# Kernel optimization log

Measured on AMD Instinct MI355X. Metric: run time of the kernel, lower is better.

The kernel has to match this reference:

```python
import jax, jax.numpy as jnp
import numpy as np

B, T, D_IN, D_FEAT, D_LAT = 256, 512, 128, 256, 512

def setup_inputs() -> dict:
    key = jax.random.key(0)
    ks = jax.random.split(key, 6)
    s = lambda fan_in: 1.0 / np.sqrt(fan_in)
    return {
        "x": jax.random.normal(ks[0], (B, T, D_IN), dtype=jnp.float32),
        "W_enc": jax.random.normal(ks[1], (D_IN, D_FEAT), dtype=jnp.float32) * s(D_IN),
        "b_enc": jnp.zeros((D_FEAT,), dtype=jnp.float32),
        "W_x": jax.random.normal(ks[2], (D_FEAT, 4 * D_LAT), dtype=jnp.float32) * s(D_FEAT),
        "W_h": jax.random.normal(ks[3], (D_LAT, 4 * D_LAT), dtype=jnp.float32) * s(D_LAT),
        "b_lstm": jnp.zeros((4 * D_LAT,), dtype=jnp.float32),
        "W_dec": jax.random.normal(ks[4], (D_LAT, 1), dtype=jnp.float32) * s(D_LAT),
        "b_dec": jnp.zeros((1,), dtype=jnp.float32),
    }

def reference(x, W_enc, b_enc, W_x, W_h, b_lstm, W_dec, b_dec):
    # Dense encoder with tanh: [B,T,D_IN] -> [B,T,D_FEAT]
    enc = jnp.tanh(jnp.einsum("bti,if->btf", x, W_enc) + b_enc)
    d = W_h.shape[0]
    # Precompute input-to-gate projection for all steps (hoisted out of loop)
    xz = jnp.einsum("btf,fg->btg", enc, W_x) + b_lstm  # [B,T,4d]
    xz_t = jnp.swapaxes(xz, 0, 1)  # [T,B,4d] for scan

    def step(carry, xz_step):
        h, c = carry
        z = xz_step + h @ W_h  # [B,4d]
        i, f, g, o = jnp.split(z, 4, axis=-1)  # Keras gate order: i,f,c,o
        i = jax.nn.sigmoid(i)
        f = jax.nn.sigmoid(f)
        g = jnp.tanh(g)
        o = jax.nn.sigmoid(o)
        c_new = f * c + i * g
        h_new = o * jnp.tanh(c_new)
        return (h_new, c_new), None

    h0 = jnp.zeros((x.shape[0], d), dtype=x.dtype)
    c0 = jnp.zeros((x.shape[0], d), dtype=x.dtype)
    (h_last, _), _ = jax.lax.scan(step, (h0, c0), xz_t)
    # Decoder on last hidden state: [B,d] -> [B,1]
    return h_last @ W_dec + b_dec
```

## Files before the change

### kernel.cpp

```cpp
#include <hip/hip_runtime.h>

#define BATCH 256
#define TLEN  512
#define DIN   128
#define DFEAT 256
#define DLAT  512
#define G4    2048
#define KCAT  768

typedef __bf16 bf16x8 __attribute__((ext_vector_type(8)));
typedef float f32x4 __attribute__((ext_vector_type(4)));

#define WCAT_OFF   0u
#define WENC_OFF   3145728u
#define ENC_OFF    3211264u
#define H_OFF      70320128u
#define FLAG_OFF   70844416u

__device__ __forceinline__ float sigf(float x)  { return 1.0f / (1.0f + __expf(-x)); }
__device__ __forceinline__ float tanhfast(float x){ return 2.0f / (1.0f + __expf(-2.0f * x)) - 1.0f; }
__device__ __forceinline__ unsigned short bfb(float f) {
    __bf16 b = (__bf16)f;
    return __builtin_bit_cast(unsigned short, b);
}

__global__ __launch_bounds__(256) void wprep_kernel(const float* __restrict__ Wx,
                                                    const float* __restrict__ Wh,
                                                    const float* __restrict__ Wenc,
                                                    __bf16* __restrict__ wcat,
                                                    __bf16* __restrict__ wencf) {
    int cid = blockIdx.x * 256 + threadIdx.x;
    float v[8];
    __bf16* dst;
    if (cid < 196608) {
        int widx = cid / 12288;
        int r1 = cid % 12288;
        int nn = r1 / 1536;
        int r2 = r1 % 1536;
        int ks = r2 >> 6, l = r2 & 63;
        int np = nn >> 1, nf = nn & 1;
        int cc = l & 15;
        int gate = (cc < 8) ? (nf ? 2 : 0) : (nf ? 3 : 1);
        int col = gate * 512 + widx * 32 + np * 8 + (cc & 7);
        int kc = ks * 32 + (l >> 4) * 8;
#pragma unroll
        for (int j = 0; j < 8; ++j) {
            int kk = kc + j;
            v[j] = (kk < DFEAT) ? Wx[kk * G4 + col] : Wh[(kk - DFEAT) * G4 + col];
        }
        dst = wcat + (size_t)cid * 8;
    } else {
        int c2 = cid - 196608;
        int ntg = c2 >> 8;
        int r = c2 & 255;
        int ks = r >> 6, l = r & 63;
        int col = ntg * 16 + (l & 15);
        int kc = ks * 32 + (l >> 4) * 8;
#pragma unroll
        for (int j = 0; j < 8; ++j) v[j] = Wenc[(kc + j) * DFEAT + col];
        dst = wencf + (size_t)c2 * 8;
    }
    bf16x8 o;
#pragma unroll
    for (int j = 0; j < 8; ++j) o[j] = (__bf16)v[j];
    *reinterpret_cast<bf16x8*>(dst) = o;
}

__global__ __launch_bounds__(256) void enc_kernel(const float* __restrict__ x,
                                                  const float* __restrict__ benc,
                                                  const __bf16* __restrict__ wencf,
                                                  __bf16* __restrict__ enc) {
    __shared__ uint4 afrag4[1024];
    __bf16* afrag = reinterpret_cast<__bf16*>(afrag4);
    int tid = threadIdx.x;
    int lane = tid & 63, w = tid >> 6;
    int rid0 = blockIdx.x * 64;
    int ntg0 = blockIdx.y * 4;

    bf16x8 wr[4][4];
#pragma unroll
    for (int n = 0; n < 4; ++n)
#pragma unroll
        for (int ks = 0; ks < 4; ++ks)
            wr[n][ks] = *reinterpret_cast<const bf16x8*>(
                wencf + (size_t)(((ntg0 + n) * 4 + ks) * 64 + lane) * 8);
    float bias[4];
#pragma unroll
    for (int n = 0; n < 4; ++n) bias[n] = benc[(ntg0 + n) * 16 + (lane & 15)];

#pragma unroll
    for (int i = 0; i < 4; ++i) {
        int c = tid + 256 * i;
        int row = c >> 4, k8 = c & 15;
        const float* src = x + (size_t)(rid0 + row) * DIN + k8 * 8;
        float4 f0 = *reinterpret_cast<const float4*>(src);
        float4 f1 = *reinterpret_cast<const float4*>(src + 4);
        bf16x8 o;
        o[0] = (__bf16)f0.x; o[1] = (__bf16)f0.y; o[2] = (__bf16)f0.z; o[3] = (__bf16)f0.w;
        o[4] = (__bf16)f1.x; o[5] = (__bf16)f1.y; o[6] = (__bf16)f1.z; o[7] = (__bf16)f1.w;
        int l = (k8 & 3) * 16 + (row & 15);
        int a16 = ((row >> 4) * 4 + (k8 >> 2)) * 64 + l;
        *reinterpret_cast<bf16x8*>(afrag + (size_t)a16 * 8) = o;
    }
    __syncthreads();

    int m = w;
    f32x4 acc[4];
#pragma unroll
    for (int n = 0; n < 4; ++n) acc[n] = (f32x4){bias[n], bias[n], bias[n], bias[n]};
#pragma unroll
    for (int ks = 0; ks < 4; ++ks) {
        bf16x8 a = *reinterpret_cast<const bf16x8*>(afrag + (size_t)((m * 4 + ks) * 64 + lane) * 8);
#pragma unroll
        for (int n = 0; n < 4; ++n)
            acc[n] = __builtin_amdgcn_mfma_f32_16x16x32_bf16(a, wr[n][ks], acc[n], 0, 0, 0);
    }
#pragma unroll
    for (int n = 0; n < 4; ++n) {
        int colg = (ntg0 + n) * 16 + (lane & 15);
#pragma unroll
        for (int q = 0; q < 4; ++q) {
            int rid = rid0 + m * 16 + (lane >> 4) * 4 + q;
            int bb = rid >> 9, tt = rid & 511;
            float th = tanhfast(acc[n][q]);
            enc[(size_t)(tt * BATCH + bb) * DFEAT + colg] = (__bf16)th;
        }
    }
}

__global__ __launch_bounds__(256, 1) void lstm_kernel(const __bf16* __restrict__ enc,
                                                      const __bf16* __restrict__ wcat,
                                                      const float* __restrict__ blstm,
                                                      __bf16* __restrict__ hbuf,
                                                      unsigned int* __restrict__ flags) {
    extern __shared__ char smem[];
    __bf16* afrag = reinterpret_cast<__bf16*>(smem);

    int tid = threadIdx.x;
    int lane = tid & 63, np = tid >> 6;
    int grp = blockIdx.x & 15, widx = blockIdx.x >> 4;
    int b0 = grp * 16;
    unsigned int* myflag = &flags[(grp * 16 + widx) * 16];

    bf16x8 wreg[2][24];
#pragma unroll
    for (int nf = 0; nf < 2; ++nf)
#pragma unroll
        for (int ks = 0; ks < 24; ++ks)
            wreg[nf][ks] = *reinterpret_cast<const bf16x8*>(
                wcat + (size_t)(((((widx * 4 + np) * 2 + nf) * 24) + ks) * 64 + lane) * 8);

    const int cbase = widx * 32 + np * 8 + (lane & 7);
    const bool lo = (lane & 15) < 8;
    const float bias0 = blstm[(lo ? 0 : 1) * 512 + cbase];
    const float bias1 = blstm[(lo ? 2 : 3) * 512 + cbase];

    float c0 = 0.f, c1 = 0.f;
    const int srow = (lane >> 4) * 4 + (lo ? 0 : 2) + (lane & 1);
    const int scol = widx * 32 + np * 8 + (lane & 6);
    unsigned* hdA = reinterpret_cast<unsigned*>(
        hbuf + (size_t)(b0 + srow) * DLAT + scol);
    unsigned* hdB = reinterpret_cast<unsigned*>(
        hbuf + (size_t)BATCH * DLAT + (size_t)(b0 + srow) * DLAT + scol);

#pragma unroll 1
    for (int t = 0; t < TLEN; ++t) {
#pragma unroll
        for (int i = 0; i < 2; ++i) {
            int c = tid + 256 * i;
            int ks = c >> 6, l = c & 63;
            int row = l & 15;
            int k = ks * 32 + (l >> 4) * 8;
            uint4 d = *reinterpret_cast<const uint4*>(
                enc + (size_t)(t * BATCH + b0 + row) * DFEAT + k);
            *reinterpret_cast<uint4*>(afrag + (size_t)c * 8) = d;
        }
        __syncthreads();

        f32x4 acc0 = (f32x4){bias0, bias0, bias0, bias0};
        f32x4 acc1 = (f32x4){bias1, bias1, bias1, bias1};
#pragma unroll
        for (int ks = 0; ks < 8; ++ks) {
            bf16x8 a = *reinterpret_cast<const bf16x8*>(
                afrag + (size_t)((ks * 64 + lane) * 8));
            acc0 = __builtin_amdgcn_mfma_f32_16x16x32_bf16(a, wreg[0][ks], acc0, 0, 0, 0);
            acc1 = __builtin_amdgcn_mfma_f32_16x16x32_bf16(a, wreg[1][ks], acc1, 0, 0, 0);
        }

        if (t > 0) {
            if (tid < 64) {
                const unsigned int* f = &flags[(grp * 16 + (lane & 15)) * 16];
                unsigned v;
                do {
                    v = __hip_atomic_load(f, __ATOMIC_RELAXED, __HIP_MEMORY_SCOPE_AGENT);
                } while (!__all((int)(v >= (unsigned)t)));
            }
            __syncthreads();

            {
                const __bf16* hsrc = hbuf + (size_t)(t & 1) * (BATCH * DLAT);
                const __bf16* src[4];
                int cdst[4];
#pragma unroll
                for (int ii = 0; ii < 4; ++ii) {
                    int c = tid + 256 * (ii + 2);
                    int ks = c >> 6, l = c & 63;
                    int row = l & 15;
                    int kh = ks * 32 + (l >> 4) * 8 - DFEAT;
                    src[ii] = hsrc + (size_t)(b0 + row) * DLAT + kh;
                    cdst[ii] = c;
                }
                uint4 d0, d1, d2, d3;
                asm volatile(
                    "global_load_dwordx4 %0, %4, off sc1\n\t"
                    "global_load_dwordx4 %1, %5, off sc1\n\t"
                    "global_load_dwordx4 %2, %6, off sc1\n\t"
                    "global_load_dwordx4 %3, %7, off sc1\n\t"
                    "s_waitcnt vmcnt(0)"
                    : "=&v"(d0), "=&v"(d1), "=&v"(d2), "=&v"(d3)
                    : "v"(src[0]), "v"(src[1]), "v"(src[2]), "v"(src[3])
                    : "memory");
                *reinterpret_cast<uint4*>(afrag + (size_t)cdst[0] * 8) = d0;
                *reinterpret_cast<uint4*>(afrag + (size_t)cdst[1] * 8) = d1;
                *reinterpret_cast<uint4*>(afrag + (size_t)cdst[2] * 8) = d2;
                *reinterpret_cast<uint4*>(afrag + (size_t)cdst[3] * 8) = d3;
            }
            __syncthreads();

#pragma unroll
            for (int ks = 8; ks < 24; ++ks) {
                bf16x8 a = *reinterpret_cast<const bf16x8*>(
                    afrag + (size_t)((ks * 64 + lane) * 8));
                acc0 = __builtin_amdgcn_mfma_f32_16x16x32_bf16(a, wreg[0][ks], acc0, 0, 0, 0);
                acc1 = __builtin_amdgcn_mfma_f32_16x16x32_bf16(a, wreg[1][ks], acc1, 0, 0, 0);
            }
        }

        float p00 = __shfl_xor(acc0[0], 8), p01 = __shfl_xor(acc0[1], 8);
        float p02 = __shfl_xor(acc0[2], 8), p03 = __shfl_xor(acc0[3], 8);
        float p10 = __shfl_xor(acc1[0], 8), p11 = __shfl_xor(acc1[1], 8);
        float p12 = __shfl_xor(acc1[2], 8), p13 = __shfl_xor(acc1[3], 8);

        float zi_a = lo ? acc0[0] : p02, zf_a = lo ? p00 : acc0[2];
        float zg_a = lo ? acc1[0] : p12, zo_a = lo ? p10 : acc1[2];
        float zi_b = lo ? acc0[1] : p03, zf_b = lo ? p01 : acc0[3];
        float zg_b = lo ? acc1[1] : p13, zo_b = lo ? p11 : acc1[3];

        float ia = sigf(zi_a), fa = sigf(zf_a), ga = tanhfast(zg_a), oa = sigf(zo_a);
        c0 = fa * c0 + ia * ga;
        float h_a = oa * tanhfast(c0);
        float ib = sigf(zi_b), fb = sigf(zf_b), gb = tanhfast(zg_b), ob = sigf(zo_b);
        c1 = fb * c1 + ib * gb;
        float h_b = ob * tanhfast(c1);

        unsigned sendv = (lane & 1) ? (unsigned)bfb(h_a) : (unsigned)bfb(h_b);
        unsigned recv = (unsigned)__shfl_xor((int)sendv, 1);
        unsigned word = (lane & 1) ? (recv | ((unsigned)bfb(h_b) << 16))
                                   : ((unsigned)bfb(h_a) | (recv << 16));
        __hip_atomic_store(((t & 1) ? hdA : hdB), word, __ATOMIC_RELAXED,
                           __HIP_MEMORY_SCOPE_AGENT);

        __syncthreads();
        if (tid == 0)
            __hip_atomic_store(myflag, (unsigned int)(t + 1), __ATOMIC_RELAXED,
                               __HIP_MEMORY_SCOPE_AGENT);
    }
}

__global__ __launch_bounds__(64) void dec_kernel(const __bf16* __restrict__ hbuf,
                                                 const float* __restrict__ wdec,
                                                 const float* __restrict__ bdec,
                                                 float* __restrict__ out) {
    int b = blockIdx.x, lane = threadIdx.x;
    uint4 d = *reinterpret_cast<const uint4*>(hbuf + (size_t)b * DLAT + lane * 8);
    const __bf16* hv = reinterpret_cast<const __bf16*>(&d);
    float4 w0 = *reinterpret_cast<const float4*>(wdec + lane * 8);
    float4 w1 = *reinterpret_cast<const float4*>(wdec + lane * 8 + 4);
    float s = (float)hv[0] * w0.x + (float)hv[1] * w0.y + (float)hv[2] * w0.z +
              (float)hv[3] * w0.w + (float)hv[4] * w1.x + (float)hv[5] * w1.y +
              (float)hv[6] * w1.z + (float)hv[7] * w1.w;
#pragma unroll
    for (int off = 32; off; off >>= 1) s += __shfl_xor(s, off);
    if (lane == 0) out[b] = s + bdec[0];
}

extern "C" void kernel_launch(void* const* d_in, const int* in_sizes, int n_in,
                              void* d_out, int out_size, void* d_ws, size_t ws_size,
                              hipStream_t stream) {
    (void)in_sizes; (void)n_in; (void)out_size; (void)ws_size;
    const float* x     = (const float*)d_in[0];
    const float* Wenc  = (const float*)d_in[1];
    const float* benc  = (const float*)d_in[2];
    const float* Wx    = (const float*)d_in[3];
    const float* Wh    = (const float*)d_in[4];
    const float* blstm = (const float*)d_in[5];
    const float* Wdec  = (const float*)d_in[6];
    const float* bdec  = (const float*)d_in[7];

    char* ws = (char*)d_ws;
    __bf16* wcat  = (__bf16*)(ws + WCAT_OFF);
    __bf16* wencf = (__bf16*)(ws + WENC_OFF);
    __bf16* enc   = (__bf16*)(ws + ENC_OFF);
    __bf16* hbuf  = (__bf16*)(ws + H_OFF);
    unsigned int* flags = (unsigned int*)(ws + FLAG_OFF);

    (void)hipMemsetAsync(ws + FLAG_OFF, 0, 16384, stream);

    wprep_kernel<<<784, 256, 0, stream>>>(Wx, Wh, Wenc, wcat, wencf);
    enc_kernel<<<dim3(2048, 4), 256, 0, stream>>>(x, benc, wencf, enc);

    (void)hipFuncSetAttribute(reinterpret_cast<const void*>(lstm_kernel),
                              hipFuncAttributeMaxDynamicSharedMemorySize, 90112);
    lstm_kernel<<<256, 256, 90112, stream>>>(enc, wcat, blstm, hbuf, flags);

    dec_kernel<<<256, 64, 0, stream>>>(hbuf, Wdec, bdec, (float*)d_out);
}
```

Baseline: 1.501 ms.

## Double-buffer encoder tiles in LDS and split MFMA accumulator chains

Prefetches the next timestep's encoder features into a second LDS buffer while the current step's MFMAs and the flag spin-wait run. This removes one barrier and the exposed global-load latency at the start of each recurrent step. It also splits each accumulator into even and odd chains to shorten MFMA dependency chains, and simplifies address math with precomputed pointers and immediate offsets. The cost is more LDS, extra accumulator registers and a final vector add.

```diff
diff --git a/kernel.cpp b/kernel.cpp
--- a/kernel.cpp
+++ b/kernel.cpp
@@ -155,6 +155,18 @@
     const float bias0 = blstm[(lo ? 0 : 1) * 512 + cbase];
     const float bias1 = blstm[(lo ? 2 : 3) * 512 + cbase];
 
+    const int srow16 = tid & 15;
+    const int kb = (tid >> 6) * 32 + ((tid >> 4) & 3) * 8;
+    const __bf16* encp = enc + (size_t)(b0 + srow16) * DFEAT + kb;
+    const __bf16* hpA = hbuf + (size_t)(b0 + srow16) * DLAT + kb;
+    const __bf16* hpB = hpA + (size_t)BATCH * DLAT;
+    __bf16* enc_ldsA = afrag + tid * 8;
+    __bf16* enc_ldsB = afrag + 4096 + tid * 8;
+    __bf16* h_lds    = afrag + 8192 + tid * 8;
+    const __bf16* aencA = afrag + lane * 8;
+    const __bf16* aencB = afrag + 4096 + lane * 8;
+    const __bf16* ah    = afrag + 8192 + lane * 8;
+
     float c0 = 0.f, c1 = 0.f;
     const int srow = (lane >> 4) * 4 + (lo ? 0 : 2) + (lane & 1);
     const int scol = widx * 32 + np * 8 + (lane & 6);
@@ -163,28 +175,39 @@
     unsigned* hdB = reinterpret_cast<unsigned*>(
         hbuf + (size_t)BATCH * DLAT + (size_t)(b0 + srow) * DLAT + scol);
 
+    {
+        uint4 e0 = *reinterpret_cast<const uint4*>(encp);
+        uint4 e1 = *reinterpret_cast<const uint4*>(encp + 128);
+        *reinterpret_cast<uint4*>(enc_ldsA) = e0;
+        *reinterpret_cast<uint4*>(enc_ldsA + 2048) = e1;
+        encp += (size_t)BATCH * DFEAT;
+    }
+    __syncthreads();
+
 #pragma unroll 1
     for (int t = 0; t < TLEN; ++t) {
-#pragma unroll
-        for (int i = 0; i < 2; ++i) {
-            int c = tid + 256 * i;
-            int ks = c >> 6, l = c & 63;
-            int row = l & 15;
-            int k = ks * 32 + (l >> 4) * 8;
-            uint4 d = *reinterpret_cast<const uint4*>(
-                enc + (size_t)(t * BATCH + b0 + row) * DFEAT + k);
-            *reinterpret_cast<uint4*>(afrag + (size_t)c * 8) = d;
-        }
-        __syncthreads();
-
-        f32x4 acc0 = (f32x4){bias0, bias0, bias0, bias0};
-        f32x4 acc1 = (f32x4){bias1, bias1, bias1, bias1};
-#pragma unroll
-        for (int ks = 0; ks < 8; ++ks) {
-            bf16x8 a = *reinterpret_cast<const bf16x8*>(
-                afrag + (size_t)((ks * 64 + lane) * 8));
-            acc0 = __builtin_amdgcn_mfma_f32_16x16x32_bf16(a, wreg[0][ks], acc0, 0, 0, 0);
-            acc1 = __builtin_amdgcn_mfma_f32_16x16x32_bf16(a, wreg[1][ks], acc1, 0, 0, 0);
+        uint4 e0, e1;
+        if (t + 1 < TLEN) {
+            asm volatile(
+                "global_load_dwordx4 %0, %2, off\n\t"
+                "global_load_dwordx4 %1, %2, off offset:256"
+                : "=&v"(e0), "=&v"(e1)
+                : "v"(encp) : "memory");
+        }
+
+        f32x4 acc0e = (f32x4){bias0, bias0, bias0, bias0};
+        f32x4 acc1e = (f32x4){bias1, bias1, bias1, bias1};
+        f32x4 acc0o = (f32x4){0.f, 0.f, 0.f, 0.f};
+        f32x4 acc1o = (f32x4){0.f, 0.f, 0.f, 0.f};
+        const __bf16* aenc = (t & 1) ? aencB : aencA;
+#pragma unroll
+        for (int ks = 0; ks < 8; ks += 2) {
+            bf16x8 a0 = *reinterpret_cast<const bf16x8*>(aenc + ks * 512);
+            bf16x8 a1 = *reinterpret_cast<const bf16x8*>(aenc + (ks + 1) * 512);
+            acc0e = __builtin_amdgcn_mfma_f32_16x16x32_bf16(a0, wreg[0][ks], acc0e, 0, 0, 0);
+            acc1e = __builtin_amdgcn_mfma_f32_16x16x32_bf16(a0, wreg[1][ks], acc1e, 0, 0, 0);
+            acc0o = __builtin_amdgcn_mfma_f32_16x16x32_bf16(a1, wreg[0][ks + 1], acc0o, 0, 0, 0);
+            acc1o = __builtin_amdgcn_mfma_f32_16x16x32_bf16(a1, wreg[1][ks + 1], acc1o, 0, 0, 0);
         }
 
         if (t > 0) {
@@ -197,54 +220,54 @@
             }
             __syncthreads();
 
-            {
-                const __bf16* hsrc = hbuf + (size_t)(t & 1) * (BATCH * DLAT);
-                const __bf16* src[4];
-                int cdst[4];
-#pragma unroll
-                for (int ii = 0; ii < 4; ++ii) {
-                    int c = tid + 256 * (ii + 2);
-                    int ks = c >> 6, l = c & 63;
-                    int row = l & 15;
-                    int kh = ks * 32 + (l >> 4) * 8 - DFEAT;
-                    src[ii] = hsrc + (size_t)(b0 + row) * DLAT + kh;
-                    cdst[ii] = c;
-                }
-                uint4 d0, d1, d2, d3;
-                asm volatile(
-                    "global_load_dwordx4 %0, %4, off sc1\n\t"
-                    "global_load_dwordx4 %1, %5, off sc1\n\t"
-                    "global_load_dwordx4 %2, %6, off sc1\n\t"
-                    "global_load_dwordx4 %3, %7, off sc1\n\t"
-                    "s_waitcnt vmcnt(0)"
-                    : "=&v"(d0), "=&v"(d1), "=&v"(d2), "=&v"(d3)
-                    : "v"(src[0]), "v"(src[1]), "v"(src[2]), "v"(src[3])
-                    : "memory");
-                *reinterpret_cast<uint4*>(afrag + (size_t)cdst[0] * 8) = d0;
-                *reinterpret_cast<uint4*>(afrag + (size_t)cdst[1] * 8) = d1;
-                *reinterpret_cast<uint4*>(afrag + (size_t)cdst[2] * 8) = d2;
-                *reinterpret_cast<uint4*>(afrag + (size_t)cdst[3] * 8) = d3;
+            const __bf16* hp = (t & 1) ? hpB : hpA;
+            uint4 d0, d1, d2, d3;
+            asm volatile(
+                "global_load_dwordx4 %0, %4, off sc1\n\t"
+                "global_load_dwordx4 %1, %4, off offset:256 sc1\n\t"
+                "global_load_dwordx4 %2, %4, off offset:512 sc1\n\t"
+                "global_load_dwordx4 %3, %4, off offset:768 sc1\n\t"
+                "s_waitcnt vmcnt(0)"
+                : "=&v"(d0), "=&v"(d1), "=&v"(d2), "=&v"(d3)
+                : "v"(hp) : "memory");
+            *reinterpret_cast<uint4*>(h_lds) = d0;
+            *reinterpret_cast<uint4*>(h_lds + 2048) = d1;
+            *reinterpret_cast<uint4*>(h_lds + 4096) = d2;
+            *reinterpret_cast<uint4*>(h_lds + 6144) = d3;
+        }
+
+        asm volatile("s_waitcnt vmcnt(0)" ::: "memory");
+        if (t + 1 < TLEN) {
+            __bf16* ed = ((t + 1) & 1) ? enc_ldsB : enc_ldsA;
+            *reinterpret_cast<uint4*>(ed) = e0;
+            *reinterpret_cast<uint4*>(ed + 2048) = e1;
+            encp += (size_t)BATCH * DFEAT;
+        }
+        __syncthreads();
+
+        if (t > 0) {
+#pragma unroll
+            for (int ks = 8; ks < 24; ks += 2) {
+                bf16x8 a0 = *reinterpret_cast<const bf16x8*>(ah + (ks - 8) * 512);
+                bf16x8 a1 = *reinterpret_cast<const bf16x8*>(ah + (ks - 7) * 512);
+                acc0e = __builtin_amdgcn_mfma_f32_16x16x32_bf16(a0, wreg[0][ks], acc0e, 0, 0, 0);
+                acc1e = __builtin_amdgcn_mfma_f32_16x16x32_bf16(a0, wreg[1][ks], acc1e, 0, 0, 0);
+                acc0o = __builtin_amdgcn_mfma_f32_16x16x32_bf16(a1, wreg[0][ks + 1], acc0o, 0, 0, 0);
+                acc1o = __builtin_amdgcn_mfma_f32_16x16x32_bf16(a1, wreg[1][ks + 1], acc1o, 0, 0, 0);
             }
-            __syncthreads();
-
-#pragma unroll
-            for (int ks = 8; ks < 24; ++ks) {
-                bf16x8 a = *reinterpret_cast<const bf16x8*>(
-                    afrag + (size_t)((ks * 64 + lane) * 8));
-                acc0 = __builtin_amdgcn_mfma_f32_16x16x32_bf16(a, wreg[0][ks], acc0, 0, 0, 0);
-                acc1 = __builtin_amdgcn_mfma_f32_16x16x32_bf16(a, wreg[1][ks], acc1, 0, 0, 0);
-            }
-        }
-
-        float p00 = __shfl_xor(acc0[0], 8), p01 = __shfl_xor(acc0[1], 8);
-        float p02 = __shfl_xor(acc0[2], 8), p03 = __shfl_xor(acc0[3], 8);
-        float p10 = __shfl_xor(acc1[0], 8), p11 = __shfl_xor(acc1[1], 8);
-        float p12 = __shfl_xor(acc1[2], 8), p13 = __shfl_xor(acc1[3], 8);
-
-        float zi_a = lo ? acc0[0] : p02, zf_a = lo ? p00 : acc0[2];
-        float zg_a = lo ? acc1[0] : p12, zo_a = lo ? p10 : acc1[2];
-        float zi_b = lo ? acc0[1] : p03, zf_b = lo ? p01 : acc0[3];
-        float zg_b = lo ? acc1[1] : p13, zo_b = lo ? p11 : acc1[3];
+        }
+        f32x4 z0 = acc0e + acc0o;
+        f32x4 z1 = acc1e + acc1o;
+
+        float p00 = __shfl_xor(z0[0], 8), p01 = __shfl_xor(z0[1], 8);
+        float p02 = __shfl_xor(z0[2], 8), p03 = __shfl_xor(z0[3], 8);
+        float p10 = __shfl_xor(z1[0], 8), p11 = __shfl_xor(z1[1], 8);
+        float p12 = __shfl_xor(z1[2], 8), p13 = __shfl_xor(z1[3], 8);
+
+        float zi_a = lo ? z0[0] : p02, zf_a = lo ? p00 : z0[2];
+        float zg_a = lo ? z1[0] : p12, zo_a = lo ? p10 : z1[2];
+        float zi_b = lo ? z0[1] : p03, zf_b = lo ? p01 : z0[3];
+        float zg_b = lo ? z1[1] : p13, zo_b = lo ? p11 : z1[3];
 
         float ia = sigf(zi_a), fa = sigf(zf_a), ga = tanhfast(zg_a), oa = sigf(zo_a);
         c0 = fa * c0 + ia * ga;
```

After: 1.273 ms. 1.18x faster.
